# Kernel tuning notes

Measured on AMD Instinct MI355X. Metric: run time of the kernel, lower is better.

## Reference

```python
import jax, jax.numpy as jnp
import numpy as np

TOL = 0.0
MARGIN = 0.0
REVERSE = False
SIZE_AVERAGE = True

N, C, H, W = 128, 256, 32, 64


def setup_inputs() -> dict:
    key = jax.random.key(0)
    k1, k2 = jax.random.split(key)
    raw_feat = jax.random.normal(k1, (N, C, H, W), dtype=jnp.float32)
    rectified_feat = jax.random.normal(k2, (N, C, H, W), dtype=jnp.float32)
    return {"raw_feat": raw_feat, "rectified_feat": rectified_feat}


def _rank(feat):
    # feat: [n, c, h, w] -> channel mean -> [n, h, w]
    n, c, h, w = feat.shape
    m = jnp.mean(feat, axis=1)                       # [n, h, w]
    flat = m.reshape(n, -1)
    nrm = jnp.linalg.norm(flat, axis=1, keepdims=True)
    normed = (flat / nrm).reshape(n, h, w)
    # batched singular values of small h x w matrices
    s = jnp.linalg.svd(normed, compute_uv=False)     # [n, min(h,w)]
    return jnp.sum((s > TOL).astype(jnp.float32), axis=1)  # [n]


def reference(raw_feat, rectified_feat):
    rank1 = _rank(raw_feat)
    rank2 = _rank(rectified_feat)
    y = jnp.full_like(rank1, -1.0 if REVERSE else 1.0)
    # margin ranking loss: max(0, -y*(x1-x2)+margin), no per-element reduction
    loss = jnp.maximum(0.0, -y * (rank1 - rank2) + MARGIN)
    if SIZE_AVERAGE:
        loss = jnp.sum(loss) / raw_feat.shape[0]
    return loss
```

## Files before the change

### kernel.cpp

```cpp
#include <hip/hip_runtime.h>
#include <math.h>


#define N_BATCH 128
#define C_CH    256
#define H_DIM   32
#define W_DIM   64
#define HW      (H_DIM * W_DIM)
#define HW4     (HW / 4)
#define PLANE4  (2 * N_BATCH * HW4)

template <int KCT>
__global__ __launch_bounds__(256) void channel_sum_part(
    const float* __restrict__ raw, const float* __restrict__ rect,
    float* __restrict__ part)
{
    int v = blockIdx.x * blockDim.x + threadIdx.x;
    int k    = v >> 17;
    int rem  = v & (PLANE4 - 1);
    int input = rem >> 16;
    int rem2  = rem & 0xFFFF;
    int n     = rem2 >> 9;
    int hw4   = rem2 & 511;

    const int CPK = C_CH / KCT;
    const float4* src = (const float4*)(input ? rect : raw);
    const float4* p = src + ((size_t)n * C_CH + (size_t)k * CPK) * HW4 + hw4;

    float4 acc = make_float4(0.f, 0.f, 0.f, 0.f);
#pragma unroll 8
    for (int c = 0; c < CPK; ++c) {
        float4 x = p[(size_t)c * HW4];
        acc.x += x.x; acc.y += x.y; acc.z += x.z; acc.w += x.w;
    }
    ((float4*)part)[(size_t)v] = acc;
}

template <int KCT>
__global__ __launch_bounds__(256) void channel_sum_reduce(float* __restrict__ part)
{
    int v = blockIdx.x * blockDim.x + threadIdx.x;
    float4* p = (float4*)part;
    float4 a = p[v];
#pragma unroll
    for (int k = 1; k < KCT; ++k) {
        float4 x = p[(size_t)k * PLANE4 + v];
        a.x += x.x; a.y += x.y; a.z += x.z; a.w += x.w;
    }
    p[v] = a;
}

__global__ __launch_bounds__(64) void rank_kernel(
    const float* __restrict__ m, float* __restrict__ ranks)
{
    int mat = blockIdx.x;
    int t   = threadIdx.x;
    const float* src = m + (size_t)mat * HW;

    float a[H_DIM];
#pragma unroll
    for (int i = 0; i < H_DIM; ++i) a[i] = src[i * W_DIM + t];

    unsigned used = 0;
    int rank = 0;
    for (int c = 0; c < W_DIM; ++c) {
        float v[H_DIM];
#pragma unroll
        for (int i = 0; i < H_DIM; ++i) v[i] = __shfl(a[i], c);

        float best = 0.0f; int p = -1;
#pragma unroll
        for (int i = 0; i < H_DIM; ++i) {
            float av = fabsf(v[i]);
            bool cand = (((used >> i) & 1u) == 0u) && (av > best);
            best = cand ? av : best;
            p    = cand ? i  : p;
        }
        if (p >= 0) {
            used |= (1u << p);
            ++rank;
            float ap = 0.0f, vp = 1.0f;
#pragma unroll
            for (int i = 0; i < H_DIM; ++i) {
                if (i == p) { ap = a[i]; vp = v[i]; }
            }
            float inv = 1.0f / vp;
#pragma unroll
            for (int i = 0; i < H_DIM; ++i) {
                if (((used >> i) & 1u) == 0u) a[i] -= (v[i] * inv) * ap;
            }
            if (rank == H_DIM) break;
        }
    }
    if (t == 0) ranks[mat] = (float)rank;
}

__global__ __launch_bounds__(128) void loss_kernel(
    const float* __restrict__ ranks, float* __restrict__ out)
{
    __shared__ float red[128];
    int t = threadIdx.x;
    float r1 = ranks[t];
    float r2 = ranks[N_BATCH + t];
    red[t] = fmaxf(0.0f, -(r1 - r2));
    __syncthreads();
    for (int s = 64; s > 0; s >>= 1) {
        if (t < s) red[t] += red[t + s];
        __syncthreads();
    }
    if (t == 0) out[0] = red[0] / (float)N_BATCH;
}

extern "C" void kernel_launch(void* const* d_in, const int* in_sizes, int n_in,
                              void* d_out, int out_size, void* d_ws, size_t ws_size,
                              hipStream_t stream)
{
    const float* raw  = (const float*)d_in[0];
    const float* rect = (const float*)d_in[1];
    float* out = (float*)d_out;

    float* part = (float*)d_ws;

    const size_t need4 = (size_t)4 * PLANE4 * 4 * sizeof(float) + 1024;
    if (ws_size >= need4) {
        float* ranks = part + (size_t)4 * PLANE4 * 4;
        channel_sum_part<4><<<(PLANE4 * 4) / 256, 256, 0, stream>>>(raw, rect, part);
        channel_sum_reduce<4><<<PLANE4 / 256, 256, 0, stream>>>(part);
        rank_kernel<<<2 * N_BATCH, 64, 0, stream>>>(part, ranks);
        loss_kernel<<<1, 128, 0, stream>>>(ranks, out);
    } else {
        float* ranks = part + (size_t)PLANE4 * 4;
        channel_sum_part<1><<<PLANE4 / 256, 256, 0, stream>>>(raw, rect, part);
        rank_kernel<<<2 * N_BATCH, 64, 0, stream>>>(part, ranks);
        loss_kernel<<<1, 128, 0, stream>>>(ranks, out);
    }
}
```

Baseline: 145.0 us.

## Fuse partial channel-sum reduction into rank kernel and restructure channel sum

Drops the separate partial-sum reduce kernel and instead sums the channel-chunk partials while loading each matrix in the rank kernel. The channel-sum kernel now assigns one block per (plane, chunk) with 512 threads and issues eight independent float4 loads per iteration for more memory-level parallelism. This saves one launch and one pass over the partial buffer. The cost is extra loads inside the small rank kernel.

Measured after the change: 144.3 us. About the same (-0.5%).

```diff
diff --git a/kernel.cpp b/kernel.cpp
--- a/kernel.cpp
+++ b/kernel.cpp
@@ -8,58 +8,59 @@
 #define W_DIM   64
 #define HW      (H_DIM * W_DIM)
 #define HW4     (HW / 4)
-#define PLANE4  (2 * N_BATCH * HW4)
 
-template <int KCT>
-__global__ __launch_bounds__(256) void channel_sum_part(
+template <int CHUNKS>
+__global__ __launch_bounds__(512) void channel_sum_kernel(
     const float* __restrict__ raw, const float* __restrict__ rect,
-    float* __restrict__ part)
+    float* __restrict__ part )
 {
-    int v = blockIdx.x * blockDim.x + threadIdx.x;
-    int k    = v >> 17;
-    int rem  = v & (PLANE4 - 1);
-    int input = rem >> 16;
-    int rem2  = rem & 0xFFFF;
-    int n     = rem2 >> 9;
-    int hw4   = rem2 & 511;
+    const int CPR = C_CH / CHUNKS;
+    int b     = blockIdx.x;
+    int chunk = b % CHUNKS;
+    int plane = b / CHUNKS;
+    int input = plane >> 7;
+    int n     = plane & 127;
 
-    const int CPK = C_CH / KCT;
-    const float4* src = (const float4*)(input ? rect : raw);
-    const float4* p = src + ((size_t)n * C_CH + (size_t)k * CPK) * HW4 + hw4;
+    const float* src = input ? rect : raw;
+    const float4* p = (const float4*)(src +
+        ((size_t)n * C_CH + (size_t)chunk * CPR) * HW) + threadIdx.x;
 
     float4 acc = make_float4(0.f, 0.f, 0.f, 0.f);
-#pragma unroll 8
-    for (int c = 0; c < CPK; ++c) {
-        float4 x = p[(size_t)c * HW4];
-        acc.x += x.x; acc.y += x.y; acc.z += x.z; acc.w += x.w;
+#pragma unroll 1
+    for (int cb = 0; cb < CPR; cb += 8) {
+        float4 x0 = p[(cb + 0) * HW4];
+        float4 x1 = p[(cb + 1) * HW4];
+        float4 x2 = p[(cb + 2) * HW4];
+        float4 x3 = p[(cb + 3) * HW4];
+        float4 x4 = p[(cb + 4) * HW4];
+        float4 x5 = p[(cb + 5) * HW4];
+        float4 x6 = p[(cb + 6) * HW4];
+        float4 x7 = p[(cb + 7) * HW4];
+        acc.x += ((x0.x + x1.x) + (x2.x + x3.x)) + ((x4.x + x5.x) + (x6.x + x7.x));
+        acc.y += ((x0.y + x1.y) + (x2.y + x3.y)) + ((x4.y + x5.y) + (x6.y + x7.y));
+        acc.z += ((x0.z + x1.z) + (x2.z + x3.z)) + ((x4.z + x5.z) + (x6.z + x7.z));
+        acc.w += ((x0.w + x1.w) + (x2.w + x3.w)) + ((x4.w + x5.w) + (x6.w + x7.w));
     }
-    ((float4*)part)[(size_t)v] = acc;
+    ((float4*)part)[(size_t)b * 512 + threadIdx.x] = acc;
 }
 
-template <int KCT>
-__global__ __launch_bounds__(256) void channel_sum_reduce(float* __restrict__ part)
-{
-    int v = blockIdx.x * blockDim.x + threadIdx.x;
-    float4* p = (float4*)part;
-    float4 a = p[v];
-#pragma unroll
-    for (int k = 1; k < KCT; ++k) {
-        float4 x = p[(size_t)k * PLANE4 + v];
-        a.x += x.x; a.y += x.y; a.z += x.z; a.w += x.w;
-    }
-    p[v] = a;
-}
-
+template <int CHUNKS>
 __global__ __launch_bounds__(64) void rank_kernel(
-    const float* __restrict__ m, float* __restrict__ ranks)
+    const float* __restrict__ part, float* __restrict__ ranks)
 {
     int mat = blockIdx.x;
     int t   = threadIdx.x;
-    const float* src = m + (size_t)mat * HW;
+    const float* base = part + (size_t)mat * CHUNKS * HW;
 
     float a[H_DIM];
 #pragma unroll
-    for (int i = 0; i < H_DIM; ++i) a[i] = src[i * W_DIM + t];
+    for (int i = 0; i < H_DIM; ++i) {
+        float s = 0.0f;
+#pragma unroll
+        for (int k = 0; k < CHUNKS; ++k)
+            s += base[k * HW + i * W_DIM + t];
+        a[i] = s;
+    }
 
     unsigned used = 0;
     int rank = 0;
@@ -118,20 +119,18 @@
     const float* raw  = (const float*)d_in[0];
     const float* rect = (const float*)d_in[1];
     float* out = (float*)d_out;
-
     float* part = (float*)d_ws;
 
-    const size_t need4 = (size_t)4 * PLANE4 * 4 * sizeof(float) + 1024;
+    const size_t need4 = (size_t)2 * N_BATCH * 4 * HW * sizeof(float) + 1024;
     if (ws_size >= need4) {
-        float* ranks = part + (size_t)4 * PLANE4 * 4;
-        channel_sum_part<4><<<(PLANE4 * 4) / 256, 256, 0, stream>>>(raw, rect, part);
-        channel_sum_reduce<4><<<PLANE4 / 256, 256, 0, stream>>>(part);
-        rank_kernel<<<2 * N_BATCH, 64, 0, stream>>>(part, ranks);
+        float* ranks = part + (size_t)2 * N_BATCH * 4 * HW;
+        channel_sum_kernel<4><<<2 * N_BATCH * 4, 512, 0, stream>>>(raw, rect, part);
+        rank_kernel<4><<<2 * N_BATCH, 64, 0, stream>>>(part, ranks);
         loss_kernel<<<1, 128, 0, stream>>>(ranks, out);
     } else {
-        float* ranks = part + (size_t)PLANE4 * 4;
-        channel_sum_part<1><<<PLANE4 / 256, 256, 0, stream>>>(raw, rect, part);
-        rank_kernel<<<2 * N_BATCH, 64, 0, stream>>>(part, ranks);
+        float* ranks = part + (size_t)2 * N_BATCH * HW;
+        channel_sum_kernel<1><<<2 * N_BATCH, 512, 0, stream>>>(raw, rect, part);
+        rank_kernel<1><<<2 * N_BATCH, 64, 0, stream>>>(part, ranks);
         loss_kernel<<<1, 128, 0, stream>>>(ranks, out);
     }
 }
```
